# Kernel tuning notes

Measured on AMD Instinct MI355X. Metric: run time of the kernel, lower is better.

## Reference

```python
import jax, jax.numpy as jnp
import numpy as np

NUM_EXPERT = 16
IN_FEAT = 1024
OUT_FEAT = 2048
N_TOKENS = 4096


def setup_inputs() -> dict:
    key = jax.random.key(0)
    k1, k2, k3 = jax.random.split(key, 3)
    x = jax.random.uniform(k1, (N_TOKENS, IN_FEAT), dtype=jnp.float32)
    gate = jax.random.randint(k2, (N_TOKENS,), 0, NUM_EXPERT, dtype=jnp.int32)
    # expert weights: [num_expert, out_feat, in_feat]
    weight = jax.random.normal(k3, (NUM_EXPERT, OUT_FEAT, IN_FEAT), dtype=jnp.float32) * 0.02
    return {"x": x, "gate": gate, "weight": weight}


def reference(x, gate, weight):
    # out[b] = weight[gate[b]] @ x[b]
    # Avoid materializing weight[gate] ([B, O, I] would be huge): scan over the
    # small, fixed expert axis with input masking (tokens not routed to expert e
    # contribute zero rows to that expert's GEMM).
    B = x.shape[0]
    E, O, I = weight.shape
    out0 = jnp.zeros((B, O), dtype=x.dtype)

    def body(out, ew):
        e, W = ew  # W: [O, I]
        xm = jnp.where((gate == e)[:, None], x, 0.0)  # [B, I] masked tokens
        return out + jnp.einsum("bi,oi->bo", xm, W), None

    out, _ = jax.lax.scan(body, out0, (jnp.arange(E), weight))
    return out
```

## Files before the change

### kernel.cpp

```cpp
#include <hip/hip_runtime.h>
#include <hip/hip_bf16.h>
#include <stdint.h>

#define N_TOKENS   4096
#define IN_FEAT    1024
#define OUT_FEAT   2048
#define NUM_EXPERT 16

#define BM 128
#define BN 128
#define BK 32
#define MAX_TILES 48
#define MAX_ROWS  6144

typedef __bf16 bf16x8 __attribute__((ext_vector_type(8)));
typedef float  f32x4  __attribute__((ext_vector_type(4)));
typedef unsigned short us8 __attribute__((ext_vector_type(8)));

__device__ __forceinline__ unsigned short f32_to_bf16_rne(float f) {
  union { float f; uint32_t u; } v; v.f = f;
  uint32_t u = v.u;
  u += 0x7fffu + ((u >> 16) & 1u);
  return (unsigned short)(u >> 16);
}

__device__ __forceinline__ void async_copy16(const void* g, void* l) {
  __builtin_amdgcn_global_load_lds(
      (const __attribute__((address_space(1))) unsigned int*)g,
      (__attribute__((address_space(3))) unsigned int*)l, 16, 0, 0);
}

__global__ void k_setup(const int* __restrict__ gate,
                        int* __restrict__ pstart,
                        int* __restrict__ tile_e,
                        int* __restrict__ tile_m,
                        int* __restrict__ row_token)
{
  __shared__ int cnt[NUM_EXPERT];
  __shared__ int cur[NUM_EXPERT];
  __shared__ int ps[NUM_EXPERT];
  const int tid = threadIdx.x;
  if (tid < NUM_EXPERT) { cnt[tid] = 0; cur[tid] = 0; }
  __syncthreads();
  for (int b = tid; b < N_TOKENS; b += 256) atomicAdd(&cnt[gate[b]], 1);
  for (int r = tid; r < MAX_ROWS; r += 256) row_token[r] = -1;
  __syncthreads();
  if (tid == 0) {
    int p = 0, tot = 0;
    for (int e = 0; e < NUM_EXPERT; ++e) {
      ps[e] = p; pstart[e] = p;
      int nt = (cnt[e] + BM - 1) / BM;
      for (int t = 0; t < nt; ++t) { tile_e[tot] = e; tile_m[tot] = t; ++tot; }
      p += nt * BM;
    }
    for (int s = tot; s < MAX_TILES; ++s) { tile_e[s] = -1; tile_m[s] = 0; }
  }
  __syncthreads();
  for (int b = tid; b < N_TOKENS; b += 256) {
    int e = gate[b];
    int pos = atomicAdd(&cur[e], 1);
    row_token[ps[e] + pos] = b;
  }
}

__global__ void k_cast_w(const float4* __restrict__ w, us8* __restrict__ wb) {
#pragma unroll
  for (int i = 0; i < 2; ++i) {
    const int p = blockIdx.x * 512 + i * 256 + threadIdx.x;
    float4 a = w[2 * p];
    float4 b = w[2 * p + 1];
    us8 o;
    o[0] = f32_to_bf16_rne(a.x); o[1] = f32_to_bf16_rne(a.y);
    o[2] = f32_to_bf16_rne(a.z); o[3] = f32_to_bf16_rne(a.w);
    o[4] = f32_to_bf16_rne(b.x); o[5] = f32_to_bf16_rne(b.y);
    o[6] = f32_to_bf16_rne(b.z); o[7] = f32_to_bf16_rne(b.w);
    wb[p] = o;
  }
}

__global__ void k_gather_x(const float4* __restrict__ x,
                           const int* __restrict__ row_token,
                           us8* __restrict__ xs) {
  const int r = blockIdx.x * 2 + (threadIdx.x >> 7);
  const int c = threadIdx.x & 127;
  const int tok = row_token[r];
  us8 o;
  if (tok >= 0) {
    float4 a = x[tok * 256 + c * 2];
    float4 b = x[tok * 256 + c * 2 + 1];
    o[0] = f32_to_bf16_rne(a.x); o[1] = f32_to_bf16_rne(a.y);
    o[2] = f32_to_bf16_rne(a.z); o[3] = f32_to_bf16_rne(a.w);
    o[4] = f32_to_bf16_rne(b.x); o[5] = f32_to_bf16_rne(b.y);
    o[6] = f32_to_bf16_rne(b.z); o[7] = f32_to_bf16_rne(b.w);
  } else {
    o = (us8)0;
  }
  xs[r * 128 + c] = o;
}

__global__ void __launch_bounds__(256)
k_gemm(const unsigned short* __restrict__ xs,
       const unsigned short* __restrict__ wb,
       const int* __restrict__ pstart,
       const int* __restrict__ tile_e,
       const int* __restrict__ tile_m,
       const int* __restrict__ row_token,
       float* __restrict__ out) {
  __shared__ unsigned short As[BM * BK];
  __shared__ unsigned short Bs[BN * BK];
  __shared__ int rowtok_s[BM];

  const int slot = blockIdx.y;
  const int e = tile_e[slot];
  if (e < 0) return;
  const int seg0 = pstart[e] + tile_m[slot] * BM;
  const int n0 = blockIdx.x * BN;

  const int tid  = threadIdx.x;
  const int wid  = tid >> 6;
  const int lane = tid & 63;
  const int lr   = lane & 15;
  const int quad = lane >> 4;
  const int wm   = (wid >> 1) * 64;
  const int wn   = (wid & 1) * 64;

  if (tid < BM) rowtok_s[tid] = row_token[seg0 + tid];

  const int srow = tid >> 2;
  const int skk  = (tid & 3) * 8;
  const unsigned short* ag = xs + (size_t)(seg0 + srow) * IN_FEAT + skk;
  const unsigned short* bg = wb + (size_t)e * OUT_FEAT * IN_FEAT
                                + (size_t)(n0 + srow) * IN_FEAT + skk;

  f32x4 acc[4][4];
  const f32x4 z = {0.f, 0.f, 0.f, 0.f};
#pragma unroll
  for (int i = 0; i < 4; ++i)
#pragma unroll
    for (int j = 0; j < 4; ++j) acc[i][j] = z;

  for (int k0 = 0; k0 < IN_FEAT; k0 += BK) {
    async_copy16(ag + k0,                &As[wid * 512]);
    async_copy16(ag + 64 * IN_FEAT + k0, &As[2048 + wid * 512]);
    async_copy16(bg + k0,                &Bs[wid * 512]);
    async_copy16(bg + 64 * IN_FEAT + k0, &Bs[2048 + wid * 512]);
    __syncthreads();

    bf16x8 af[4], bf[4];
#pragma unroll
    for (int mi = 0; mi < 4; ++mi)
      af[mi] = *(const bf16x8*)&As[(wm + mi * 16 + lr) * BK + quad * 8];
#pragma unroll
    for (int ni = 0; ni < 4; ++ni)
      bf[ni] = *(const bf16x8*)&Bs[(wn + ni * 16 + lr) * BK + quad * 8];
#pragma unroll
    for (int mi = 0; mi < 4; ++mi)
#pragma unroll
      for (int ni = 0; ni < 4; ++ni)
        acc[mi][ni] = __builtin_amdgcn_mfma_f32_16x16x32_bf16(
            af[mi], bf[ni], acc[mi][ni], 0, 0, 0);
    __syncthreads();
  }

#pragma unroll
  for (int mi = 0; mi < 4; ++mi) {
    const int mb = wm + mi * 16 + quad * 4;
    const int t0 = rowtok_s[mb + 0];
    const int t1 = rowtok_s[mb + 1];
    const int t2 = rowtok_s[mb + 2];
    const int t3 = rowtok_s[mb + 3];
#pragma unroll
    for (int ni = 0; ni < 4; ++ni) {
      const int n = n0 + wn + ni * 16 + lr;
      f32x4 c = acc[mi][ni];
      if (t0 >= 0) out[(size_t)t0 * OUT_FEAT + n] = c[0];
      if (t1 >= 0) out[(size_t)t1 * OUT_FEAT + n] = c[1];
      if (t2 >= 0) out[(size_t)t2 * OUT_FEAT + n] = c[2];
      if (t3 >= 0) out[(size_t)t3 * OUT_FEAT + n] = c[3];
    }
  }
}

extern "C" void kernel_launch(void* const* d_in, const int* in_sizes, int n_in,
                              void* d_out, int out_size, void* d_ws, size_t ws_size,
                              hipStream_t stream) {
  const float* x    = (const float*)d_in[0];
  const int*   gate = (const int*)d_in[1];
  const float* w    = (const float*)d_in[2];
  float* out = (float*)d_out;

  char* ws = (char*)d_ws;
  unsigned short* wb = (unsigned short*)ws;
  unsigned short* xs = (unsigned short*)(ws + 67108864);
  int* row_token = (int*)(ws + 67108864 + 12582912);
  int* pstart = row_token + MAX_ROWS;
  int* tile_e = pstart + NUM_EXPERT;
  int* tile_m = tile_e + MAX_TILES;

  k_setup<<<1, 256, 0, stream>>>(gate, pstart, tile_e, tile_m, row_token);
  k_cast_w<<<8192, 256, 0, stream>>>((const float4*)w, (us8*)wb);
  k_gather_x<<<MAX_ROWS / 2, 256, 0, stream>>>((const float4*)x, row_token,
                                               (us8*)xs);
  dim3 g(OUT_FEAT / BN, MAX_TILES);
  k_gemm<<<g, 256, 0, stream>>>(xs, wb, pstart, tile_e, tile_m, row_token, out);
}
```

Baseline: 284.9 us.

## Fuse fp32-to-bf16 weight cast into GEMM tile loading

Removes the separate weight-cast kernel and has the GEMM load fp32 weights directly, converting them to bf16 in registers before storing to shared memory. This avoids a full pass writing and rereading a bf16 copy of all expert weights. In exchange, each m-tile rereads fp32 weights (twice the bytes) and the B-tile load becomes a synchronous register load instead of an async global-to-LDS copy.

```diff
diff --git a/kernel.cpp b/kernel.cpp
--- a/kernel.cpp
+++ b/kernel.cpp
@@ -63,21 +63,6 @@
   }
 }
 
-__global__ void k_cast_w(const float4* __restrict__ w, us8* __restrict__ wb) {
-#pragma unroll
-  for (int i = 0; i < 2; ++i) {
-    const int p = blockIdx.x * 512 + i * 256 + threadIdx.x;
-    float4 a = w[2 * p];
-    float4 b = w[2 * p + 1];
-    us8 o;
-    o[0] = f32_to_bf16_rne(a.x); o[1] = f32_to_bf16_rne(a.y);
-    o[2] = f32_to_bf16_rne(a.z); o[3] = f32_to_bf16_rne(a.w);
-    o[4] = f32_to_bf16_rne(b.x); o[5] = f32_to_bf16_rne(b.y);
-    o[6] = f32_to_bf16_rne(b.z); o[7] = f32_to_bf16_rne(b.w);
-    wb[p] = o;
-  }
-}
-
 __global__ void k_gather_x(const float4* __restrict__ x,
                            const int* __restrict__ row_token,
                            us8* __restrict__ xs) {
@@ -100,7 +85,7 @@
 
 __global__ void __launch_bounds__(256)
 k_gemm(const unsigned short* __restrict__ xs,
-       const unsigned short* __restrict__ wb,
+       const float* __restrict__ w,
        const int* __restrict__ pstart,
        const int* __restrict__ tile_e,
        const int* __restrict__ tile_m,
@@ -129,8 +114,13 @@
   const int srow = tid >> 2;
   const int skk  = (tid & 3) * 8;
   const unsigned short* ag = xs + (size_t)(seg0 + srow) * IN_FEAT + skk;
-  const unsigned short* bg = wb + (size_t)e * OUT_FEAT * IN_FEAT
-                                + (size_t)(n0 + srow) * IN_FEAT + skk;
+
+  const int brow = tid >> 1;
+  const int bk16 = (tid & 1) * 16;
+  const float* bg = w + (size_t)e * OUT_FEAT * IN_FEAT
+                      + (size_t)(n0 + brow) * IN_FEAT + bk16;
+  us8* bs0 = (us8*)&Bs[brow * BK + bk16];
+  us8* bs1 = (us8*)&Bs[brow * BK + bk16 + 8];
 
   f32x4 acc[4][4];
   const f32x4 z = {0.f, 0.f, 0.f, 0.f};
@@ -140,10 +130,21 @@
     for (int j = 0; j < 4; ++j) acc[i][j] = z;
 
   for (int k0 = 0; k0 < IN_FEAT; k0 += BK) {
+    const float4* bp = (const float4*)(bg + k0);
+    float4 f0 = bp[0], f1 = bp[1], f2 = bp[2], f3 = bp[3];
     async_copy16(ag + k0,                &As[wid * 512]);
     async_copy16(ag + 64 * IN_FEAT + k0, &As[2048 + wid * 512]);
-    async_copy16(bg + k0,                &Bs[wid * 512]);
-    async_copy16(bg + 64 * IN_FEAT + k0, &Bs[2048 + wid * 512]);
+    us8 lo, hi;
+    lo[0] = f32_to_bf16_rne(f0.x); lo[1] = f32_to_bf16_rne(f0.y);
+    lo[2] = f32_to_bf16_rne(f0.z); lo[3] = f32_to_bf16_rne(f0.w);
+    lo[4] = f32_to_bf16_rne(f1.x); lo[5] = f32_to_bf16_rne(f1.y);
+    lo[6] = f32_to_bf16_rne(f1.z); lo[7] = f32_to_bf16_rne(f1.w);
+    hi[0] = f32_to_bf16_rne(f2.x); hi[1] = f32_to_bf16_rne(f2.y);
+    hi[2] = f32_to_bf16_rne(f2.z); hi[3] = f32_to_bf16_rne(f2.w);
+    hi[4] = f32_to_bf16_rne(f3.x); hi[5] = f32_to_bf16_rne(f3.y);
+    hi[6] = f32_to_bf16_rne(f3.z); hi[7] = f32_to_bf16_rne(f3.w);
+    *bs0 = lo;
+    *bs1 = hi;
     __syncthreads();
 
     bf16x8 af[4], bf[4];
@@ -190,17 +191,15 @@
   float* out = (float*)d_out;
 
   char* ws = (char*)d_ws;
-  unsigned short* wb = (unsigned short*)ws;
-  unsigned short* xs = (unsigned short*)(ws + 67108864);
-  int* row_token = (int*)(ws + 67108864 + 12582912);
+  unsigned short* xs = (unsigned short*)ws;
+  int* row_token = (int*)(ws + 12582912);
   int* pstart = row_token + MAX_ROWS;
   int* tile_e = pstart + NUM_EXPERT;
   int* tile_m = tile_e + MAX_TILES;
 
   k_setup<<<1, 256, 0, stream>>>(gate, pstart, tile_e, tile_m, row_token);
-  k_cast_w<<<8192, 256, 0, stream>>>((const float4*)w, (us8*)wb);
   k_gather_x<<<MAX_ROWS / 2, 256, 0, stream>>>((const float4*)x, row_token,
                                                (us8*)xs);
   dim3 g(OUT_FEAT / BN, MAX_TILES);
-  k_gemm<<<g, 256, 0, stream>>>(xs, wb, pstart, tile_e, tile_m, row_token, out);
-}
+  k_gemm<<<g, 256, 0, stream>>>(xs, w, pstart, tile_e, tile_m, row_token, out);
+}
```

Result: faster. 271.1 us (-4.8%).
